# Kernel tuning notes

Measured on AMD Instinct MI355X. Metric: run time of the kernel, lower is better.

## Reference

```python
import jax, jax.numpy as jnp
import numpy as np

B, N, M, D = 8, 2048, 2048, 512

def setup_inputs() -> dict:
    key = jax.random.key(0)
    ks = jax.random.split(key, 10)
    s = 1.0 / np.sqrt(D)  # torch Linear default init scale (approx)
    return {
        "lidar_features": jax.random.normal(ks[0], (B, N, D), jnp.float32),
        "camera_features": jax.random.normal(ks[1], (B, M, D), jnp.float32),
        "lidar_confidence": jax.random.uniform(ks[2], (B, N, 1), jnp.float32),
        "camera_confidence": jax.random.uniform(ks[3], (B, M, 1), jnp.float32),
        "Wq": jax.random.normal(ks[4], (D, D), jnp.float32) * s,
        "bq": jnp.zeros((D,), jnp.float32),
        "Wk": jax.random.normal(ks[5], (D, D), jnp.float32) * s,
        "bk": jnp.zeros((D,), jnp.float32),
        "Wv": jax.random.normal(ks[6], (D, D), jnp.float32) * s,
        "bv": jnp.zeros((D,), jnp.float32),
    }

def reference(lidar_features, camera_features, lidar_confidence, camera_confidence,
              Wq, bq, Wk, bk, Wv, bv):
    # torch nn.Linear: x @ W.T + b
    q = (jnp.einsum('bnd,ed->bne', lidar_features, Wq) + bq) * lidar_confidence
    k = jnp.einsum('bmd,ed->bme', camera_features, Wk) + bk
    v = jnp.einsum('bmd,ed->bme', camera_features, Wv) + bv
    # note: no 1/sqrt(d) scaling in the original; camera_confidence is unused
    scores = jnp.einsum('bne,bme->bnm', q, k)  # [B,N,M]
    attn = jax.nn.softmax(scores, axis=-1)
    fused = jnp.einsum('bnm,bme->bne', attn, v)
    return fused
```

## Files before the change

### kernel.cpp

```cpp
#include <hip/hip_runtime.h>
#include <hip/hip_bf16.h>

#define BB 8
#define NN 2048
#define MM 2048
#define DD 512

typedef __attribute__((ext_vector_type(8))) _Float16 f16x8;
typedef __attribute__((ext_vector_type(4))) float f32x4;
typedef __attribute__((ext_vector_type(8))) unsigned short u16x8;

__device__ __forceinline__ unsigned short f2h(float x){
  union { _Float16 h; unsigned short u; } cv;
  cv.h = (_Float16)x;
  return cv.u;
}
__device__ __forceinline__ f32x4 mfmah(f16x8 a, f16x8 b, f32x4 c){
  return __builtin_amdgcn_mfma_f32_16x16x32_f16(a, b, c, 0, 0, 0);
}

__device__ __forceinline__ void swz_xyz(int& bn, int& bm, int& bz){
  int f = ((int)blockIdx.z * (int)gridDim.y + (int)blockIdx.y) * (int)gridDim.x
        + (int)blockIdx.x;
  bz = f & 7;
  int r = f >> 3;
  bn = r % (int)gridDim.x;
  bm = r / (int)gridDim.x;
}

__global__ __launch_bounds__(256) void cvt16_kernel(const float* __restrict__ in,
    unsigned short* __restrict__ out, int n4){
  int i = blockIdx.x*256 + threadIdx.x;
  const int stride = gridDim.x*256;
  for (; i < n4; i += stride){
    float4 v = ((const float4*)in)[i];
    ushort4 h; h.x=f2h(v.x); h.y=f2h(v.y); h.z=f2h(v.z); h.w=f2h(v.w);
    ((ushort4*)out)[i] = h;
  }
}

__global__ __launch_bounds__(256) void cam_prep(const float* __restrict__ cam,
    const float* __restrict__ c2,
    unsigned short* __restrict__ camH,
    float* __restrict__ svec){
  const int t = threadIdx.x;
  const int l = t & 63;
  const size_t row = (size_t)blockIdx.x*4 + (t >> 6);
  const float4* r4 = (const float4*)(cam + row*DD);
  const float4* c4 = (const float4*)c2;
  float4 v0 = r4[l*2],   v1 = r4[l*2+1];
  float4 a0 = c4[l*2],   a1 = c4[l*2+1];
  float p = v0.x*a0.x + v0.y*a0.y + v0.z*a0.z + v0.w*a0.w
          + v1.x*a1.x + v1.y*a1.y + v1.z*a1.z + v1.w*a1.w;
  for (int o = 32; o; o >>= 1) p += __shfl_xor(p, o);
  if (l == 0) svec[row] = p;
  ushort4 h0; h0.x=f2h(v0.x); h0.y=f2h(v0.y); h0.z=f2h(v0.z); h0.w=f2h(v0.w);
  ushort4 h1; h1.x=f2h(v1.x); h1.y=f2h(v1.y); h1.z=f2h(v1.z); h1.w=f2h(v1.w);
  ushort4* dst = (ushort4*)(camH + row*DD);
  dst[l*2]   = h0;
  dst[l*2+1] = h1;
}

__global__ __launch_bounds__(256) void at_kernel(const float* __restrict__ Wq,
                                                 const float* __restrict__ Wk,
                                                 unsigned short* __restrict__ atH){
  const int i0 = blockIdx.x * 32, j0 = blockIdx.y * 32;
  __shared__ float q_s[32][33];
  __shared__ float k_s[32][33];
  const int t = threadIdx.x;
  const int tx = t & 15, ty = t >> 4;
  float acc[2][2] = {{0.f,0.f},{0.f,0.f}};
  for (int e0 = 0; e0 < DD; e0 += 32){
    __syncthreads();
#pragma unroll
    for (int p = 0; p < 4; ++p){
      int idx = t + 256*p;
      int e = idx >> 5, c = idx & 31;
      q_s[e][c] = Wq[(size_t)(e0+e)*DD + i0 + c];
      k_s[e][c] = Wk[(size_t)(e0+e)*DD + j0 + c];
    }
    __syncthreads();
#pragma unroll 8
    for (int e = 0; e < 32; ++e){
      float q0 = q_s[e][2*tx], q1 = q_s[e][2*tx+1];
      float k0 = k_s[e][2*ty], k1 = k_s[e][2*ty+1];
      acc[0][0] += k0*q0; acc[0][1] += k0*q1;
      acc[1][0] += k1*q0; acc[1][1] += k1*q1;
    }
  }
#pragma unroll
  for (int a = 0; a < 2; ++a)
#pragma unroll
    for (int b = 0; b < 2; ++b)
      atH[(size_t)(j0 + 2*ty + a)*DD + i0 + 2*tx + b] = f2h(acc[a][b]);
}

__global__ __launch_bounds__(256) void c2_kernel(const float* __restrict__ bq,
                                                 const float* __restrict__ Wk,
                                                 float* __restrict__ c2){
  int d = blockIdx.x * 256 + threadIdx.x;
  float a = 0.f;
  for (int e = 0; e < DD; ++e) a += bq[e] * Wk[(size_t)e*DD + d];
  c2[d] = a;
}

template<int MODE>
__global__ __launch_bounds__(256) void gemm_h128(
    const unsigned short* __restrict__ Ag, long sA, int lda,
    const unsigned short* __restrict__ Bg, long sB, int ldb,
    unsigned short* __restrict__ O, long sO, int ldo,
    const float* __restrict__ bias)
{
  __shared__ __attribute__((aligned(16))) unsigned short Ah[128][40];
  __shared__ __attribute__((aligned(16))) unsigned short Bh[128][40];

  int bn, bm, bz; swz_xyz(bn, bm, bz);
  const int t = threadIdx.x;
  const int lane = t & 63, w = t >> 6;
  const int wrow = w >> 1, wcol = w & 1;
  const int lr = lane & 15, lk = (lane >> 4) << 3;

  f32x4 acc[4][4];
#pragma unroll
  for (int m = 0; m < 4; ++m)
#pragma unroll
    for (int n = 0; n < 4; ++n){ f32x4 z = {0.f,0.f,0.f,0.f}; acc[m][n] = z; }

  const unsigned short* Ap = Ag + (size_t)bz*(size_t)sA + ((size_t)bm*128)*(size_t)lda;
  const unsigned short* Bp = Bg + (size_t)bz*(size_t)sB + ((size_t)bn*128)*(size_t)ldb;

  const int sr = t >> 2;
  const int sc = (t & 3) * 8;

  for (int k0 = 0; k0 < DD; k0 += 32){
    __syncthreads();
#pragma unroll
    for (int p = 0; p < 2; ++p){
      int r = sr + 64*p;
      *(u16x8*)&Ah[r][sc] = *(const u16x8*)(Ap + (size_t)r*lda + k0 + sc);
      *(u16x8*)&Bh[r][sc] = *(const u16x8*)(Bp + (size_t)r*ldb + k0 + sc);
    }
    __syncthreads();

    f16x8 af[4], bf[4];
#pragma unroll
    for (int m = 0; m < 4; ++m) af[m] = *(const f16x8*)&Ah[wrow*64 + m*16 + lr][lk];
#pragma unroll
    for (int n = 0; n < 4; ++n) bf[n] = *(const f16x8*)&Bh[wcol*64 + n*16 + lr][lk];
#pragma unroll
    for (int m = 0; m < 4; ++m)
#pragma unroll
      for (int n = 0; n < 4; ++n)
        acc[m][n] = mfmah(af[m], bf[n], acc[m][n]);
  }

  const int orow = bm*128 + wrow*64;
  const int ocol = bn*128 + wcol*64;
#pragma unroll
  for (int m = 0; m < 4; ++m){
#pragma unroll
    for (int n = 0; n < 4; ++n){
      int col  = ocol + n*16 + lr;
      int row0 = orow + m*16 + ((lane >> 4) << 2);
#pragma unroll
      for (int r = 0; r < 4; ++r){
        int row = row0 + r;
        float v = acc[m][n][r];
        if constexpr (MODE == 1) v += bias[row];
        O[(size_t)bz*(size_t)sO + (size_t)row*ldo + col] = f2h(v);
      }
    }
  }
}

__global__ __launch_bounds__(512) void gemm_scores(
    const unsigned short* __restrict__ Th, const unsigned short* __restrict__ camH,
    float* __restrict__ O,
    const float* __restrict__ conf, const float* __restrict__ svec)
{
  __shared__ __attribute__((aligned(16))) unsigned short Ah[128][40];
  __shared__ __attribute__((aligned(16))) unsigned short Bh[256][40];

  int bn, bm, bz; swz_xyz(bn, bm, bz);
  const int t = threadIdx.x;
  const int lane = t & 63, w = t >> 6;
  const int wrow = w >> 2, wcol = w & 3;
  const int lr = lane & 15, lk = (lane >> 4) << 3;

  f32x4 acc[4][4];
#pragma unroll
  for (int m = 0; m < 4; ++m)
#pragma unroll
    for (int n = 0; n < 4; ++n){ f32x4 z = {0.f,0.f,0.f,0.f}; acc[m][n] = z; }

  const unsigned short* Ap = Th   + (size_t)bz*((size_t)NN*DD) + ((size_t)bm*128)*DD;
  const unsigned short* Bp = camH + (size_t)bz*((size_t)MM*DD) + ((size_t)bn*256)*DD;

  const int sr = t >> 2;
  const int sc = (t & 3) * 8;

  for (int k0 = 0; k0 < DD; k0 += 32){
    __syncthreads();
    *(u16x8*)&Ah[sr][sc] = *(const u16x8*)(Ap + (size_t)sr*DD + k0 + sc);
#pragma unroll
    for (int p = 0; p < 2; ++p){
      int r = sr + 128*p;
      *(u16x8*)&Bh[r][sc] = *(const u16x8*)(Bp + (size_t)r*DD + k0 + sc);
    }
    __syncthreads();

    f16x8 af[4], bf[4];
#pragma unroll
    for (int m = 0; m < 4; ++m) af[m] = *(const f16x8*)&Ah[wrow*64 + m*16 + lr][lk];
#pragma unroll
    for (int n = 0; n < 4; ++n) bf[n] = *(const f16x8*)&Bh[wcol*64 + n*16 + lr][lk];
#pragma unroll
    for (int m = 0; m < 4; ++m)
#pragma unroll
      for (int n = 0; n < 4; ++n)
        acc[m][n] = mfmah(af[m], bf[n], acc[m][n]);
  }

  const int orow0 = bm*128 + wrow*64;
  const int ocol0 = bn*256 + wcol*64;
  const size_t obase = (size_t)bz*((size_t)NN*MM);
#pragma unroll
  for (int m = 0; m < 4; ++m){
#pragma unroll
    for (int n = 0; n < 4; ++n){
      int col  = ocol0 + n*16 + lr;
      float sv = svec[bz*MM + col];
      int row0 = orow0 + m*16 + ((lane >> 4) << 2);
#pragma unroll
      for (int r = 0; r < 4; ++r){
        int row = row0 + r;
        O[obase + (size_t)row*MM + col]
            = conf[bz*NN + row] * (acc[m][n][r] + sv);
      }
    }
  }
}

__global__ __launch_bounds__(512) void gemm_pv(
    const unsigned short* __restrict__ P,
    const unsigned short* __restrict__ V,
    float* __restrict__ O)
{
  __shared__ __attribute__((aligned(16))) unsigned short Ah[64][40];
  __shared__ __attribute__((aligned(16))) unsigned short Bh[256][40];

  int bn, bm, bz; swz_xyz(bn, bm, bz);
  const int t = threadIdx.x;
  const int lane = t & 63, w = t >> 6;
  const int lr = lane & 15, lk = (lane >> 4) << 3;

  f32x4 acc[4][2];
#pragma unroll
  for (int m = 0; m < 4; ++m)
#pragma unroll
    for (int n = 0; n < 2; ++n){ f32x4 z = {0.f,0.f,0.f,0.f}; acc[m][n] = z; }

  const unsigned short* Ap = P + (size_t)bz*((size_t)NN*2*MM) + ((size_t)bm*64)*(2*MM);
  const unsigned short* Bp = V + (size_t)bz*((size_t)DD*MM) + ((size_t)bn*256)*MM;

  for (int k0 = 0; k0 < MM; k0 += 32){
    __syncthreads();
    if (t < 256){
      int sr = t >> 2, sc = (t & 3) * 8;
      *(u16x8*)&Ah[sr][sc] = *(const u16x8*)(Ap + (size_t)sr*(2*MM) + k0 + sc);
    }
#pragma unroll
    for (int p = 0; p < 2; ++p){
      int slot = t + 512*p;
      int r = slot >> 2, sc = (slot & 3) * 8;
      *(u16x8*)&Bh[r][sc] = *(const u16x8*)(Bp + (size_t)r*MM + k0 + sc);
    }
    __syncthreads();

    f16x8 af[4], bf[2];
#pragma unroll
    for (int m = 0; m < 4; ++m) af[m] = *(const f16x8*)&Ah[m*16 + lr][lk];
#pragma unroll
    for (int n = 0; n < 2; ++n) bf[n] = *(const f16x8*)&Bh[w*32 + n*16 + lr][lk];
#pragma unroll
    for (int m = 0; m < 4; ++m)
#pragma unroll
      for (int n = 0; n < 2; ++n)
        acc[m][n] = mfmah(af[m], bf[n], acc[m][n]);
  }

  const int orow0 = bm*64;
  const int ocol0 = bn*256 + w*32;
#pragma unroll
  for (int m = 0; m < 4; ++m){
#pragma unroll
    for (int n = 0; n < 2; ++n){
      int col  = ocol0 + n*16 + lr;
      int row0 = orow0 + m*16 + ((lane >> 4) << 2);
#pragma unroll
      for (int r = 0; r < 4; ++r){
        int row = row0 + r;
        O[(size_t)bz*((size_t)NN*DD) + (size_t)row*DD + col] = acc[m][n][r];
      }
    }
  }
}

__global__ __launch_bounds__(256) void softmax_kernel(float* __restrict__ scores){
  const size_t row = blockIdx.x;
  float* src = scores + row * MM;
  unsigned short* dst = (unsigned short*)scores + row * (size_t)(2*MM);
  const int t = threadIdx.x;

  float4 v0 = ((const float4*)src)[t];
  float4 v1 = ((const float4*)src)[t + 256];

  float mx = fmaxf(fmaxf(fmaxf(v0.x,v0.y), fmaxf(v0.z,v0.w)),
                   fmaxf(fmaxf(v1.x,v1.y), fmaxf(v1.z,v1.w)));
  for (int o = 32; o; o >>= 1) mx = fmaxf(mx, __shfl_xor(mx, o));
  __shared__ float red[4];
  if ((t & 63) == 0) red[t >> 6] = mx;
  __syncthreads();
  mx = fmaxf(fmaxf(red[0], red[1]), fmaxf(red[2], red[3]));

  float e0x = __expf(v0.x - mx), e0y = __expf(v0.y - mx);
  float e0z = __expf(v0.z - mx), e0w = __expf(v0.w - mx);
  float e1x = __expf(v1.x - mx), e1y = __expf(v1.y - mx);
  float e1z = __expf(v1.z - mx), e1w = __expf(v1.w - mx);
  float s = e0x+e0y+e0z+e0w+e1x+e1y+e1z+e1w;
  for (int o = 32; o; o >>= 1) s += __shfl_xor(s, o);
  __syncthreads();
  if ((t & 63) == 0) red[t >> 6] = s;
  __syncthreads();
  float inv = 1.f / (red[0] + red[1] + red[2] + red[3]);

  ushort4 p0; p0.x=f2h(e0x*inv); p0.y=f2h(e0y*inv); p0.z=f2h(e0z*inv); p0.w=f2h(e0w*inv);
  ushort4 p1; p1.x=f2h(e1x*inv); p1.y=f2h(e1y*inv); p1.z=f2h(e1z*inv); p1.w=f2h(e1w*inv);
  ((ushort4*)dst)[t]       = p0;
  ((ushort4*)dst)[t + 256] = p1;
}

extern "C" void kernel_launch(void* const* d_in, const int* in_sizes, int n_in,
                              void* d_out, int out_size, void* d_ws, size_t ws_size,
                              hipStream_t stream) {
  const float* lidar  = (const float*)d_in[0];
  const float* camera = (const float*)d_in[1];
  const float* lconf  = (const float*)d_in[2];
  const float* Wq = (const float*)d_in[4];
  const float* bq = (const float*)d_in[5];
  const float* Wk = (const float*)d_in[6];
  const float* Wv = (const float*)d_in[8];
  const float* bv = (const float*)d_in[9];
  float* out = (float*)d_out;

  char* ws = (char*)d_ws;
  float*          scores = (float*)(ws + 0);
  unsigned short* liH    = (unsigned short*)(ws + 0);
  unsigned short* atH    = (unsigned short*)(ws + 16777216);
  unsigned short* wvH    = (unsigned short*)(ws + 17301504);
  float*          c2     = (float*)(ws + 17825792);
  unsigned short* Th     = (unsigned short*)(ws + 134217728);
  unsigned short* camH   = (unsigned short*)(ws + 150994944);
  unsigned short* Vt     = (unsigned short*)(ws + 167772160);
  float*          svec   = (float*)(ws + 184549376);

  c2_kernel<<<dim3(2), 256, 0, stream>>>(bq, Wk, c2);
  cam_prep<<<dim3(BB*MM/4), 256, 0, stream>>>(camera, c2, camH, svec);
  cvt16_kernel<<<dim3(2048), 256, 0, stream>>>(lidar,  liH,  BB*NN*DD/4);
  cvt16_kernel<<<dim3(256),  256, 0, stream>>>(Wv,     wvH,  DD*DD/4);
  at_kernel<<<dim3(16,16), 256, 0, stream>>>(Wq, Wk, atH);

  gemm_h128<0><<<dim3(DD/128, NN/128, BB), 256, 0, stream>>>(
      liH, (long)NN*DD, DD,  atH, 0, DD,
      Th, (long)NN*DD, DD, nullptr);

  gemm_h128<1><<<dim3(MM/128, DD/128, BB), 256, 0, stream>>>(
      wvH, 0, DD,  camH, (long)MM*DD, DD,
      Vt, (long)DD*MM, MM, bv);

  gemm_scores<<<dim3(MM/256, NN/128, BB), 512, 0, stream>>>(
      Th, camH, scores, lconf, svec);

  softmax_kernel<<<dim3(BB*NN), 256, 0, stream>>>(scores);

  gemm_pv<<<dim3(DD/256, NN/64, BB), 512, 0, stream>>>(
      (const unsigned short*)scores, Vt, out);
}
```

Baseline: 243.4 us.

## Double-buffer PV GEMM with direct global-to-LDS loads and XOR swizzle

Rewrites the P·V GEMM main loop to use double-buffered LDS tiles filled by global_load_lds direct copies, so the next K-tile loads while MFMAs run on the current one. K-step grows from 32 to 64, and an XOR swizzle on the 16-byte chunk index replaces padding to avoid LDS bank conflicts. The loop now has one barrier per iteration, and MFMA issue gets raised priority via setprio. The trade-offs are more LDS use, which may lower occupancy, and manual waitcnt/barrier handling that has to be exactly right.

```diff
diff --git a/kernel.cpp b/kernel.cpp
--- a/kernel.cpp
+++ b/kernel.cpp
@@ -18,6 +18,12 @@
 __device__ __forceinline__ f32x4 mfmah(f16x8 a, f16x8 b, f32x4 c){
   return __builtin_amdgcn_mfma_f32_16x16x32_f16(a, b, c, 0, 0, 0);
 }
+
+#define GLD16(gp, lp) __builtin_amdgcn_global_load_lds( \
+    (const __attribute__((address_space(1))) void*)(gp), \
+    (__attribute__((address_space(3))) void*)(lp), 16, 0, 0)
+
+#define WAITVM(n) __builtin_amdgcn_s_waitcnt(0xF70 | (n))
 
 __device__ __forceinline__ void swz_xyz(int& bn, int& bm, int& bz){
   int f = ((int)blockIdx.z * (int)gridDim.y + (int)blockIdx.y) * (int)gridDim.x
@@ -246,48 +252,80 @@
     const unsigned short* __restrict__ V,
     float* __restrict__ O)
 {
-  __shared__ __attribute__((aligned(16))) unsigned short Ah[64][40];
-  __shared__ __attribute__((aligned(16))) unsigned short Bh[256][40];
+  __shared__ unsigned short Ah[2][64][64];
+  __shared__ unsigned short Bh[2][256][64];
 
   int bn, bm, bz; swz_xyz(bn, bm, bz);
   const int t = threadIdx.x;
   const int lane = t & 63, w = t >> 6;
-  const int lr = lane & 15, lk = (lane >> 4) << 3;
-
-  f32x4 acc[4][2];
-#pragma unroll
-  for (int m = 0; m < 4; ++m)
-#pragma unroll
-    for (int n = 0; n < 2; ++n){ f32x4 z = {0.f,0.f,0.f,0.f}; acc[m][n] = z; }
+  const int lr = lane & 15, lc0 = lane >> 4;
 
   const unsigned short* Ap = P + (size_t)bz*((size_t)NN*2*MM) + ((size_t)bm*64)*(2*MM);
   const unsigned short* Bp = V + (size_t)bz*((size_t)DD*MM) + ((size_t)bn*256)*MM;
 
-  for (int k0 = 0; k0 < MM; k0 += 32){
-    __syncthreads();
-    if (t < 256){
-      int sr = t >> 2, sc = (t & 3) * 8;
-      *(u16x8*)&Ah[sr][sc] = *(const u16x8*)(Ap + (size_t)sr*(2*MM) + k0 + sc);
-    }
-#pragma unroll
-    for (int p = 0; p < 2; ++p){
-      int slot = t + 512*p;
-      int r = slot >> 2, sc = (slot & 3) * 8;
-      *(u16x8*)&Bh[r][sc] = *(const u16x8*)(Bp + (size_t)r*MM + k0 + sc);
-    }
-    __syncthreads();
-
-    f16x8 af[4], bf[2];
-#pragma unroll
-    for (int m = 0; m < 4; ++m) af[m] = *(const f16x8*)&Ah[m*16 + lr][lk];
-#pragma unroll
-    for (int n = 0; n < 2; ++n) bf[n] = *(const f16x8*)&Bh[w*32 + n*16 + lr][lk];
+  const int arow = 8*w + (lane >> 3);
+  const int alc  = (lane & 7) ^ (arow & 7);
+  const unsigned short* gA = Ap + (size_t)arow*(2*MM) + alc*8;
+  const int brow = 32*w + (lane >> 3);
+  const int blc  = (lane & 7) ^ (brow & 7);
+  const unsigned short* gB = Bp + (size_t)brow*MM + blc*8;
+
+#define PV_STAGE(bufi, kofs) do {                                   \
+    GLD16(gA + (kofs),                 &Ah[bufi][8*w][0]);          \
+    GLD16(gB + (kofs),                 &Bh[bufi][32*w     ][0]);    \
+    GLD16(gB + (kofs) + (size_t)8*MM,  &Bh[bufi][32*w +  8][0]);    \
+    GLD16(gB + (kofs) + (size_t)16*MM, &Bh[bufi][32*w + 16][0]);    \
+    GLD16(gB + (kofs) + (size_t)24*MM, &Bh[bufi][32*w + 24][0]);    \
+  } while(0)
+
+  f32x4 acc[4][2];
+#pragma unroll
+  for (int m = 0; m < 4; ++m)
+#pragma unroll
+    for (int n = 0; n < 2; ++n){ f32x4 z = {0.f,0.f,0.f,0.f}; acc[m][n] = z; }
+
+  PV_STAGE(0, 0);
+  WAITVM(0);
+  __builtin_amdgcn_s_barrier();
+  __builtin_amdgcn_sched_barrier(0);
+
+  for (int tt = 0; tt < 32; ++tt){
+    const int buf = tt & 1;
+    if (tt < 31) PV_STAGE(buf^1, (size_t)(tt+1)*64);
+    f16x8 af[4][2], bf[2][2];
+#pragma unroll
+    for (int m = 0; m < 4; ++m){
+      int row = m*16 + lr;
+#pragma unroll
+      for (int ks = 0; ks < 2; ++ks){
+        int pc = (ks*4 + lc0) ^ (row & 7);
+        af[m][ks] = *(const f16x8*)&Ah[buf][row][pc*8];
+      }
+    }
+#pragma unroll
+    for (int n = 0; n < 2; ++n){
+      int row = w*32 + n*16 + lr;
+#pragma unroll
+      for (int ks = 0; ks < 2; ++ks){
+        int pc = (ks*4 + lc0) ^ (row & 7);
+        bf[n][ks] = *(const f16x8*)&Bh[buf][row][pc*8];
+      }
+    }
+    __builtin_amdgcn_s_setprio(1);
 #pragma unroll
     for (int m = 0; m < 4; ++m)
 #pragma unroll
-      for (int n = 0; n < 2; ++n)
-        acc[m][n] = mfmah(af[m], bf[n], acc[m][n]);
-  }
+      for (int n = 0; n < 2; ++n){
+        acc[m][n] = mfmah(af[m][0], bf[n][0], acc[m][n]);
+        acc[m][n] = mfmah(af[m][1], bf[n][1], acc[m][n]);
+      }
+    __builtin_amdgcn_s_setprio(0);
+
+    WAITVM(0);
+    __builtin_amdgcn_s_barrier();
+    __builtin_amdgcn_sched_barrier(0);
+  }
+#undef PV_STAGE
 
   const int orow0 = bm*64;
   const int ocol0 = bn*256 + w*32;
```

Result: faster. 221.3 us (-9.1%).

## Fuse scores, softmax and PV into a single online-softmax flash kernel

Applied to the files above, without the earlier changes.

Replaces the three-kernel chain (fp32 score GEMM, row softmax, PV GEMM) with one flash-attention style kernel. Each block holds 64 query rows in LDS, double-buffers camera key tiles via global_load_lds, and keeps a running max and sum per row. This avoids writing and re-reading the full B×N×M score matrix in HBM. In exchange it runs only 256 blocks of 8 waves, uses a serial MFMA chain per tile, needs several barriers per key tile, and loads V fragments straight from global memory.

```diff
diff --git a/kernel.cpp b/kernel.cpp
--- a/kernel.cpp
+++ b/kernel.cpp
@@ -18,6 +18,12 @@
 __device__ __forceinline__ f32x4 mfmah(f16x8 a, f16x8 b, f32x4 c){
   return __builtin_amdgcn_mfma_f32_16x16x32_f16(a, b, c, 0, 0, 0);
 }
+
+#define GLD16(gp, lp) __builtin_amdgcn_global_load_lds( \
+    (const __attribute__((address_space(1))) void*)(gp), \
+    (__attribute__((address_space(3))) void*)(lp), 16, 0, 0)
+
+#define WAITVM(n) __builtin_amdgcn_s_waitcnt(0xF70 | (n))
 
 __device__ __forceinline__ void swz_xyz(int& bn, int& bm, int& bz){
   int f = ((int)blockIdx.z * (int)gridDim.y + (int)blockIdx.y) * (int)gridDim.x
@@ -173,171 +179,168 @@
   }
 }
 
-__global__ __launch_bounds__(512) void gemm_scores(
-    const unsigned short* __restrict__ Th, const unsigned short* __restrict__ camH,
-    float* __restrict__ O,
-    const float* __restrict__ conf, const float* __restrict__ svec)
-{
-  __shared__ __attribute__((aligned(16))) unsigned short Ah[128][40];
-  __shared__ __attribute__((aligned(16))) unsigned short Bh[256][40];
-
-  int bn, bm, bz; swz_xyz(bn, bm, bz);
-  const int t = threadIdx.x;
-  const int lane = t & 63, w = t >> 6;
-  const int wrow = w >> 2, wcol = w & 3;
-  const int lr = lane & 15, lk = (lane >> 4) << 3;
-
-  f32x4 acc[4][4];
-#pragma unroll
-  for (int m = 0; m < 4; ++m)
-#pragma unroll
-    for (int n = 0; n < 4; ++n){ f32x4 z = {0.f,0.f,0.f,0.f}; acc[m][n] = z; }
-
-  const unsigned short* Ap = Th   + (size_t)bz*((size_t)NN*DD) + ((size_t)bm*128)*DD;
-  const unsigned short* Bp = camH + (size_t)bz*((size_t)MM*DD) + ((size_t)bn*256)*DD;
-
-  const int sr = t >> 2;
-  const int sc = (t & 3) * 8;
-
-  for (int k0 = 0; k0 < DD; k0 += 32){
-    __syncthreads();
-    *(u16x8*)&Ah[sr][sc] = *(const u16x8*)(Ap + (size_t)sr*DD + k0 + sc);
-#pragma unroll
-    for (int p = 0; p < 2; ++p){
-      int r = sr + 128*p;
-      *(u16x8*)&Bh[r][sc] = *(const u16x8*)(Bp + (size_t)r*DD + k0 + sc);
-    }
-    __syncthreads();
-
-    f16x8 af[4], bf[4];
-#pragma unroll
-    for (int m = 0; m < 4; ++m) af[m] = *(const f16x8*)&Ah[wrow*64 + m*16 + lr][lk];
-#pragma unroll
-    for (int n = 0; n < 4; ++n) bf[n] = *(const f16x8*)&Bh[wcol*64 + n*16 + lr][lk];
-#pragma unroll
-    for (int m = 0; m < 4; ++m)
-#pragma unroll
-      for (int n = 0; n < 4; ++n)
-        acc[m][n] = mfmah(af[m], bf[n], acc[m][n]);
-  }
-
-  const int orow0 = bm*128 + wrow*64;
-  const int ocol0 = bn*256 + wcol*64;
-  const size_t obase = (size_t)bz*((size_t)NN*MM);
-#pragma unroll
-  for (int m = 0; m < 4; ++m){
-#pragma unroll
-    for (int n = 0; n < 4; ++n){
-      int col  = ocol0 + n*16 + lr;
-      float sv = svec[bz*MM + col];
-      int row0 = orow0 + m*16 + ((lane >> 4) << 2);
-#pragma unroll
-      for (int r = 0; r < 4; ++r){
-        int row = row0 + r;
-        O[obase + (size_t)row*MM + col]
-            = conf[bz*NN + row] * (acc[m][n][r] + sv);
-      }
-    }
-  }
-}
-
-__global__ __launch_bounds__(512) void gemm_pv(
-    const unsigned short* __restrict__ P,
-    const unsigned short* __restrict__ V,
+__global__ __launch_bounds__(512) void flash_kernel(
+    const unsigned short* __restrict__ Th,
+    const unsigned short* __restrict__ camH,
+    const unsigned short* __restrict__ Vt,
+    const float* __restrict__ conf,
+    const float* __restrict__ svec,
     float* __restrict__ O)
 {
-  __shared__ __attribute__((aligned(16))) unsigned short Ah[64][40];
-  __shared__ __attribute__((aligned(16))) unsigned short Bh[256][40];
-
-  int bn, bm, bz; swz_xyz(bn, bm, bz);
-  const int t = threadIdx.x;
-  const int lane = t & 63, w = t >> 6;
-  const int lr = lane & 15, lk = (lane >> 4) << 3;
-
-  f32x4 acc[4][2];
-#pragma unroll
-  for (int m = 0; m < 4; ++m)
-#pragma unroll
-    for (int n = 0; n < 2; ++n){ f32x4 z = {0.f,0.f,0.f,0.f}; acc[m][n] = z; }
-
-  const unsigned short* Ap = P + (size_t)bz*((size_t)NN*2*MM) + ((size_t)bm*64)*(2*MM);
-  const unsigned short* Bp = V + (size_t)bz*((size_t)DD*MM) + ((size_t)bn*256)*MM;
-
-  for (int k0 = 0; k0 < MM; k0 += 32){
-    __syncthreads();
-    if (t < 256){
-      int sr = t >> 2, sc = (t & 3) * 8;
-      *(u16x8*)&Ah[sr][sc] = *(const u16x8*)(Ap + (size_t)sr*(2*MM) + k0 + sc);
-    }
-#pragma unroll
-    for (int p = 0; p < 2; ++p){
-      int slot = t + 512*p;
-      int r = slot >> 2, sc = (slot & 3) * 8;
-      *(u16x8*)&Bh[r][sc] = *(const u16x8*)(Bp + (size_t)r*MM + k0 + sc);
-    }
-    __syncthreads();
-
-    f16x8 af[4], bf[2];
-#pragma unroll
-    for (int m = 0; m < 4; ++m) af[m] = *(const f16x8*)&Ah[m*16 + lr][lk];
-#pragma unroll
-    for (int n = 0; n < 2; ++n) bf[n] = *(const f16x8*)&Bh[w*32 + n*16 + lr][lk];
-#pragma unroll
-    for (int m = 0; m < 4; ++m)
-#pragma unroll
-      for (int n = 0; n < 2; ++n)
-        acc[m][n] = mfmah(af[m], bf[n], acc[m][n]);
-  }
-
-  const int orow0 = bm*64;
-  const int ocol0 = bn*256 + w*32;
-#pragma unroll
-  for (int m = 0; m < 4; ++m){
-#pragma unroll
-    for (int n = 0; n < 2; ++n){
-      int col  = ocol0 + n*16 + lr;
-      int row0 = orow0 + m*16 + ((lane >> 4) << 2);
-#pragma unroll
-      for (int r = 0; r < 4; ++r){
-        int row = row0 + r;
-        O[(size_t)bz*((size_t)NN*DD) + (size_t)row*DD + col] = acc[m][n][r];
+  __shared__ unsigned short T_s[64][520];
+  __shared__ unsigned short cam_s[2][32][520];
+  __shared__ unsigned short P_s[64][40];
+  __shared__ float redm[2][64], reds[2][64], resc_s[64];
+  __shared__ float mrun[64], lrun[64], conf_s[64];
+
+  const int f  = (int)blockIdx.y * 32 + (int)blockIdx.x;
+  const int bz = f & 7;
+  const int nb = f >> 3;
+  const int t = threadIdx.x, lane = t & 63, w = t >> 6;
+  const int r = w >> 1, c = w & 1;
+  const int g = lane >> 4, l15 = lane & 15;
+
+  const unsigned short* Tg   = Th   + ((size_t)bz*NN + (size_t)nb*64)*DD;
+  const unsigned short* camg = camH + (size_t)bz*((size_t)MM*DD);
+  const unsigned short* Vtg  = Vt   + (size_t)bz*((size_t)DD*MM);
+
+#pragma unroll
+  for (int j = 0; j < 8; ++j){
+    int idx = j*512 + t;
+    int row = idx >> 6, ch = idx & 63;
+    *(u16x8*)&T_s[row][ch*8] = *(const u16x8*)(Tg + (size_t)row*DD + ch*8);
+  }
+  if (t < 64){
+    mrun[t] = -3.0e38f; lrun[t] = 0.f;
+    conf_s[t] = conf[bz*NN + nb*64 + t];
+  }
+
+#define STAGECAM(bufi, m0_) do {                                            \
+    _Pragma("unroll")                                                       \
+    for (int j = 0; j < 4; ++j)                                             \
+      GLD16(camg + (size_t)((m0_) + 4*w + j)*DD + lane*8,                   \
+            &cam_s[bufi][4*w + j][0]);                                      \
+  } while(0)
+
+  STAGECAM(0, 0);
+  WAITVM(0);
+  __syncthreads();
+
+  f32x4 acc[4][4];
+#pragma unroll
+  for (int nf = 0; nf < 4; ++nf)
+#pragma unroll
+    for (int ef = 0; ef < 4; ++ef){ f32x4 z = {0.f,0.f,0.f,0.f}; acc[nf][ef] = z; }
+
+  for (int mt = 0; mt < 64; ++mt){
+    const int m0 = mt*32;
+    const int buf = mt & 1;
+    if (mt < 63) STAGECAM(buf^1, m0+32);
+    f16x8 bf[4];
+#pragma unroll
+    for (int ef = 0; ef < 4; ++ef)
+      bf[ef] = *(const f16x8*)(Vtg + (size_t)(w*64 + ef*16 + l15)*MM + m0 + g*8);
+    const float sv = svec[bz*MM + m0 + c*16 + l15];
+
+    f32x4 sacc = {0.f,0.f,0.f,0.f};
+#pragma unroll
+    for (int kk = 0; kk < 16; ++kk){
+      f16x8 a = *(const f16x8*)&T_s[r*16 + l15][kk*32 + g*8];
+      f16x8 b = *(const f16x8*)&cam_s[buf][c*16 + l15][kk*32 + g*8];
+      sacc = mfmah(a, b, sacc);
+    }
+
+    float s0 = conf_s[r*16 + g*4 + 0] * (sacc[0] + sv);
+    float s1 = conf_s[r*16 + g*4 + 1] * (sacc[1] + sv);
+    float s2 = conf_s[r*16 + g*4 + 2] * (sacc[2] + sv);
+    float s3 = conf_s[r*16 + g*4 + 3] * (sacc[3] + sv);
+    float m0_ = s0, m1_ = s1, m2_ = s2, m3_ = s3;
+#pragma unroll
+    for (int msk = 1; msk <= 8; msk <<= 1){
+      m0_ = fmaxf(m0_, __shfl_xor(m0_, msk));
+      m1_ = fmaxf(m1_, __shfl_xor(m1_, msk));
+      m2_ = fmaxf(m2_, __shfl_xor(m2_, msk));
+      m3_ = fmaxf(m3_, __shfl_xor(m3_, msk));
+    }
+    if (l15 == 0){
+      redm[c][r*16 + g*4 + 0] = m0_;
+      redm[c][r*16 + g*4 + 1] = m1_;
+      redm[c][r*16 + g*4 + 2] = m2_;
+      redm[c][r*16 + g*4 + 3] = m3_;
+    }
+    __syncthreads();
+    if (t < 64){
+      float nm = fmaxf(mrun[t], fmaxf(redm[0][t], redm[1][t]));
+      resc_s[t] = __expf(mrun[t] - nm);
+      mrun[t] = nm;
+    }
+    __syncthreads();
+    float p0 = __expf(s0 - mrun[r*16 + g*4 + 0]);
+    float p1 = __expf(s1 - mrun[r*16 + g*4 + 1]);
+    float p2 = __expf(s2 - mrun[r*16 + g*4 + 2]);
+    float p3 = __expf(s3 - mrun[r*16 + g*4 + 3]);
+    float q0 = p0, q1 = p1, q2 = p2, q3 = p3;
+#pragma unroll
+    for (int msk = 1; msk <= 8; msk <<= 1){
+      q0 += __shfl_xor(q0, msk);
+      q1 += __shfl_xor(q1, msk);
+      q2 += __shfl_xor(q2, msk);
+      q3 += __shfl_xor(q3, msk);
+    }
+    if (l15 == 0){
+      reds[c][r*16 + g*4 + 0] = q0;
+      reds[c][r*16 + g*4 + 1] = q1;
+      reds[c][r*16 + g*4 + 2] = q2;
+      reds[c][r*16 + g*4 + 3] = q3;
+    }
+    P_s[r*16 + g*4 + 0][c*16 + l15] = f2h(p0);
+    P_s[r*16 + g*4 + 1][c*16 + l15] = f2h(p1);
+    P_s[r*16 + g*4 + 2][c*16 + l15] = f2h(p2);
+    P_s[r*16 + g*4 + 3][c*16 + l15] = f2h(p3);
+#pragma unroll
+    for (int nf = 0; nf < 4; ++nf){
+      float rs0 = resc_s[nf*16 + g*4 + 0];
+      float rs1 = resc_s[nf*16 + g*4 + 1];
+      float rs2 = resc_s[nf*16 + g*4 + 2];
+      float rs3 = resc_s[nf*16 + g*4 + 3];
+#pragma unroll
+      for (int ef = 0; ef < 4; ++ef){
+        acc[nf][ef][0] *= rs0; acc[nf][ef][1] *= rs1;
+        acc[nf][ef][2] *= rs2; acc[nf][ef][3] *= rs3;
       }
     }
-  }
-}
-
-__global__ __launch_bounds__(256) void softmax_kernel(float* __restrict__ scores){
-  const size_t row = blockIdx.x;
-  float* src = scores + row * MM;
-  unsigned short* dst = (unsigned short*)scores + row * (size_t)(2*MM);
-  const int t = threadIdx.x;
-
-  float4 v0 = ((const float4*)src)[t];
-  float4 v1 = ((const float4*)src)[t + 256];
-
-  float mx = fmaxf(fmaxf(fmaxf(v0.x,v0.y), fmaxf(v0.z,v0.w)),
-                   fmaxf(fmaxf(v1.x,v1.y), fmaxf(v1.z,v1.w)));
-  for (int o = 32; o; o >>= 1) mx = fmaxf(mx, __shfl_xor(mx, o));
-  __shared__ float red[4];
-  if ((t & 63) == 0) red[t >> 6] = mx;
+    WAITVM(0);
+    __syncthreads();
+    if (t < 64) lrun[t] = lrun[t]*resc_s[t] + reds[0][t] + reds[1][t];
+    f16x8 af[4];
+#pragma unroll
+    for (int nf = 0; nf < 4; ++nf)
+      af[nf] = *(const f16x8*)&P_s[nf*16 + l15][g*8];
+#pragma unroll
+    for (int nf = 0; nf < 4; ++nf)
+#pragma unroll
+      for (int ef = 0; ef < 4; ++ef)
+        acc[nf][ef] = mfmah(af[nf], bf[ef], acc[nf][ef]);
+  }
+#undef STAGECAM
+
   __syncthreads();
-  mx = fmaxf(fmaxf(red[0], red[1]), fmaxf(red[2], red[3]));
-
-  float e0x = __expf(v0.x - mx), e0y = __expf(v0.y - mx);
-  float e0z = __expf(v0.z - mx), e0w = __expf(v0.w - mx);
-  float e1x = __expf(v1.x - mx), e1y = __expf(v1.y - mx);
-  float e1z = __expf(v1.z - mx), e1w = __expf(v1.w - mx);
-  float s = e0x+e0y+e0z+e0w+e1x+e1y+e1z+e1w;
-  for (int o = 32; o; o >>= 1) s += __shfl_xor(s, o);
-  __syncthreads();
-  if ((t & 63) == 0) red[t >> 6] = s;
-  __syncthreads();
-  float inv = 1.f / (red[0] + red[1] + red[2] + red[3]);
-
-  ushort4 p0; p0.x=f2h(e0x*inv); p0.y=f2h(e0y*inv); p0.z=f2h(e0z*inv); p0.w=f2h(e0w*inv);
-  ushort4 p1; p1.x=f2h(e1x*inv); p1.y=f2h(e1y*inv); p1.z=f2h(e1z*inv); p1.w=f2h(e1w*inv);
-  ((ushort4*)dst)[t]       = p0;
-  ((ushort4*)dst)[t + 256] = p1;
+  float* Og = O + ((size_t)bz*NN + (size_t)nb*64)*DD;
+#pragma unroll
+  for (int nf = 0; nf < 4; ++nf){
+    float i0 = 1.f / lrun[nf*16 + g*4 + 0];
+    float i1 = 1.f / lrun[nf*16 + g*4 + 1];
+    float i2 = 1.f / lrun[nf*16 + g*4 + 2];
+    float i3 = 1.f / lrun[nf*16 + g*4 + 3];
+#pragma unroll
+    for (int ef = 0; ef < 4; ++ef){
+      int col = w*64 + ef*16 + l15;
+      Og[(size_t)(nf*16 + g*4 + 0)*DD + col] = acc[nf][ef][0] * i0;
+      Og[(size_t)(nf*16 + g*4 + 1)*DD + col] = acc[nf][ef][1] * i1;
+      Og[(size_t)(nf*16 + g*4 + 2)*DD + col] = acc[nf][ef][2] * i2;
+      Og[(size_t)(nf*16 + g*4 + 3)*DD + col] = acc[nf][ef][3] * i3;
+    }
+  }
 }
 
 extern "C" void kernel_launch(void* const* d_in, const int* in_sizes, int n_in,
@@ -354,7 +357,6 @@
   float* out = (float*)d_out;
 
   char* ws = (char*)d_ws;
-  float*          scores = (float*)(ws + 0);
   unsigned short* liH    = (unsigned short*)(ws + 0);
   unsigned short* atH    = (unsigned short*)(ws + 16777216);
   unsigned short* wvH    = (unsigned short*)(ws + 17301504);
@@ -378,11 +380,6 @@
       wvH, 0, DD,  camH, (long)MM*DD, DD,
       Vt, (long)DD*MM, MM, bv);
 
-  gemm_scores<<<dim3(MM/256, NN/128, BB), 512, 0, stream>>>(
-      Th, camH, scores, lconf, svec);
-
-  softmax_kernel<<<dim3(BB*NN), 256, 0, stream>>>(scores);
-
-  gemm_pv<<<dim3(DD/256, NN/64, BB), 512, 0, stream>>>(
-      (const unsigned short*)scores, Vt, out);
-}
+  flash_kernel<<<dim3(32, 8), 512, 0, stream>>>(
+      Th, camH, Vt, lconf, svec, out);
+}
```

Measured after the change: 271.6 us. +11.6%, slower.
